# Kernel optimization log

Measured on AMD Instinct MI355X. Metric: run time of the kernel, lower is better.

Reference implementation:

```python
import jax, jax.numpy as jnp
import numpy as np
from jax import lax

EPS = 1e-5
SLOPE = 0.2

def knn_idx(x, k):
    # x: [B, C, N] -> neighbor indices [B, N, k] (largest negative sq-dist, self included)
    inner = jnp.einsum('bcn,bcm->bnm', x, x)          # [B,N,N]
    xx = jnp.sum(x * x, axis=1)                        # [B,N]
    pair = 2.0 * inner - xx[:, :, None] - xx[:, None, :]
    return lax.top_k(pair, k)[1]                       # [B,N,k]

def graph_feature(x, idx):
    # x: [B,C,N], idx: [B,N,k] -> edge features [B,N,k,2C] = (x_j - x_i, x_i)
    feat = jnp.transpose(x, (0, 2, 1))                 # [B,N,C]
    nbr = jax.vmap(lambda f, i: f[i])(feat, idx)       # [B,N,k,C]
    ctr = jnp.broadcast_to(feat[:, :, None, :], nbr.shape)
    return jnp.concatenate([nbr - ctr, ctr], axis=-1)  # [B,N,k,2C]

def bn(x, gamma, beta, axes):
    mu = jnp.mean(x, axis=axes, keepdims=True)
    var = jnp.var(x, axis=axes, keepdims=True)
    return (x - mu) * lax.rsqrt(var + EPS) * gamma + beta

def edge_conv(e, w, gamma, beta):
    # e: [B,N,k,2C], w: [O,2C] (1x1 conv, no bias) -> [B,N,O] after BN+LeakyReLU+max over k
    h = jnp.einsum('bnkc,oc->bnko', e, w)
    h = jax.nn.leaky_relu(bn(h, gamma, beta, (0, 1, 2)), SLOPE)
    return jnp.max(h, axis=2)                          # [B,N,O]

def setup_inputs() -> dict:
    key = jax.random.key(0)
    ks = jax.random.split(key, 8)
    B, C, N, O = 8, 3, 4096, 64
    x = jax.random.normal(ks[0], (B, C, N), jnp.float32)
    w_s = jax.random.normal(ks[1], (O, 2 * C), jnp.float32) * (1.0 / np.sqrt(2 * C))
    w_l = jax.random.normal(ks[2], (O, 2 * C), jnp.float32) * (1.0 / np.sqrt(2 * C))
    w_f = jax.random.normal(ks[3], (O, 2 * O), jnp.float32) * (1.0 / np.sqrt(2 * O))
    g_s = jnp.ones((O,)); b_s = jnp.zeros((O,))
    g_l = jnp.ones((O,)); b_l = jnp.zeros((O,))
    g_f = jnp.ones((O,)); b_f = jnp.zeros((O,))
    return {"x": x, "w_s": w_s, "g_s": g_s, "b_s": b_s,
            "w_l": w_l, "g_l": g_l, "b_l": b_l,
            "w_f": w_f, "g_f": g_f, "b_f": b_f}

def reference(x, w_s, g_s, b_s, w_l, g_l, b_l, w_f, g_f, b_f):
    K_SMALL, K_LARGE = 20, 40
    idx_s = knn_idx(x, K_SMALL)
    idx_l = knn_idx(x, K_LARGE)
    h_s = edge_conv(graph_feature(x, idx_s), w_s, g_s, b_s)   # [B,N,O]
    h_l = edge_conv(graph_feature(x, idx_l), w_l, g_l, b_l)   # [B,N,O]
    h = jnp.concatenate([h_s, h_l], axis=-1)                  # [B,N,2O]
    h = jnp.einsum('bnc,oc->bno', h, w_f)                     # fuse 1x1 conv
    h = jax.nn.leaky_relu(bn(h, g_f, b_f, (0, 1)), SLOPE)
    return jnp.transpose(h, (0, 2, 1))                        # [B,O,N]
```

## Files before the change

kernel.cpp:

```cpp
#include <hip/hip_runtime.h>

#define B_ 8
#define N_ 4096
#define O_ 64
#define KL 40
#define KS 20
#define EPSV 1e-5
#define SLOPE 0.2f

typedef unsigned long long u64;
typedef unsigned int u32;

__device__ __forceinline__ float leaky(float v) { return v >= 0.f ? v : SLOPE * v; }

__device__ __forceinline__ u32 mfloat(float x) {
    const u32 u = __float_as_uint(x);
    return (u & 0x80000000u) ? ~u : (u | 0x80000000u);
}
__device__ __forceinline__ float unmfloat(u32 m) {
    return __uint_as_float((m & 0x80000000u) ? (m ^ 0x80000000u) : ~m);
}

template <int S>
__device__ __forceinline__ u64 xor_ex64(u64 v, int dsaddr) {
    if constexpr (S == 1 || S == 2 || S == 8) {
        constexpr int CTRL = (S == 1) ? 0xB1 : (S == 2) ? 0x4E : 0x128;
        const int lo = __builtin_amdgcn_update_dpp(0, (int)(u32)v, CTRL, 0xF, 0xF, true);
        const int hi = __builtin_amdgcn_update_dpp(0, (int)(u32)(v >> 32), CTRL, 0xF, 0xF, true);
        return ((u64)(u32)hi << 32) | (u32)lo;
    } else {
        const int lo = __builtin_amdgcn_ds_bpermute(dsaddr, (int)(u32)v);
        const int hi = __builtin_amdgcn_ds_bpermute(dsaddr, (int)(u32)(v >> 32));
        return ((u64)(u32)hi << 32) | (u32)lo;
    }
}

template <int K, int S>
__device__ __forceinline__ void stage_pair(u64& a, u64& e, int lane, int dsaddr) {
    const u64 oa = xor_ex64<S>(a, dsaddr);
    const u64 oe = xor_ex64<S>(e, dsaddr);
    const bool sel = (((lane & K) == 0) == ((lane & S) == 0));
    a = ((a < oa) == sel) ? a : oa;
    e = ((e < oe) == sel) ? e : oe;
}

__device__ __forceinline__ void sort64_pair(u64& a, u64& e, int lane,
                                            int a4, int a16, int a32) {
    stage_pair<2, 1>(a, e, lane, 0);
    stage_pair<4, 2>(a, e, lane, 0);    stage_pair<4, 1>(a, e, lane, 0);
    stage_pair<8, 4>(a, e, lane, a4);   stage_pair<8, 2>(a, e, lane, 0);    stage_pair<8, 1>(a, e, lane, 0);
    stage_pair<16, 8>(a, e, lane, 0);   stage_pair<16, 4>(a, e, lane, a4);  stage_pair<16, 2>(a, e, lane, 0);   stage_pair<16, 1>(a, e, lane, 0);
    stage_pair<32, 16>(a, e, lane, a16); stage_pair<32, 8>(a, e, lane, 0);  stage_pair<32, 4>(a, e, lane, a4);  stage_pair<32, 2>(a, e, lane, 0);  stage_pair<32, 1>(a, e, lane, 0);
    stage_pair<64, 32>(a, e, lane, a32); stage_pair<64, 16>(a, e, lane, a16); stage_pair<64, 8>(a, e, lane, 0); stage_pair<64, 4>(a, e, lane, a4); stage_pair<64, 2>(a, e, lane, 0); stage_pair<64, 1>(a, e, lane, 0);
}

__device__ __forceinline__ void merge_pair(u64& L0, u64& L1, u64 a, u64 e, int lane,
                                           int a4, int a16, int a32, int a63) {
    const u64 ra = xor_ex64<63>(a, a63);
    const u64 re = xor_ex64<63>(e, a63);
    L0 = (L0 < ra) ? L0 : ra;
    L1 = (L1 < re) ? L1 : re;
    stage_pair<0, 32>(L0, L1, lane, a32);
    stage_pair<0, 16>(L0, L1, lane, a16);
    stage_pair<0, 8>(L0, L1, lane, 0);
    stage_pair<0, 4>(L0, L1, lane, a4);
    stage_pair<0, 2>(L0, L1, lane, 0);
    stage_pair<0, 1>(L0, L1, lane, 0);
}

__global__ __launch_bounds__(1024) void bucket_kernel(const float* __restrict__ x,
                                                      float4* __restrict__ sxp,
                                                      int* __restrict__ perm,
                                                      float2* __restrict__ cb,
                                                      float4* __restrict__ xo4) {
    __shared__ int hist[256];
    __shared__ int scan[256];
    __shared__ int ofs[256];
    __shared__ u32 xsm[4096];
    __shared__ float redmin[16], redmax[16];
    __shared__ u32 wmin[64], wmax[64];
    const int b = blockIdx.x;
    const float* xb = x + (size_t)b * 3 * N_;
    const int t = threadIdx.x;
    float xv[4];
    float mn = INFINITY, mx = -INFINITY;
#pragma unroll
    for (int p = 0; p < 4; ++p) {
        xv[p] = xb[t + p * 1024];
        mn = fminf(mn, xv[p]); mx = fmaxf(mx, xv[p]);
    }
#pragma unroll
    for (int s = 1; s < 64; s <<= 1) {
        mn = fminf(mn, __shfl_xor(mn, s));
        mx = fmaxf(mx, __shfl_xor(mx, s));
    }
    if ((t & 63) == 0) { redmin[t >> 6] = mn; redmax[t >> 6] = mx; }
    if (t < 256) hist[t] = 0;
    __syncthreads();
    if (t == 0) {
        float m0 = INFINITY, m1 = -INFINITY;
        for (int w = 0; w < 16; ++w) { m0 = fminf(m0, redmin[w]); m1 = fmaxf(m1, redmax[w]); }
        redmin[0] = m0; redmax[0] = m1;
    }
    __syncthreads();
    const float xmin = redmin[0];
    const float scale = 256.0f / fmaxf(redmax[0] - xmin, 1e-20f);
    int bk[4];
#pragma unroll
    for (int p = 0; p < 4; ++p) {
        bk[p] = min(255, max(0, (int)((xv[p] - xmin) * scale)));
        atomicAdd(&hist[bk[p]], 1);
    }
    __syncthreads();
    if (t < 256) scan[t] = hist[t];
    __syncthreads();
#pragma unroll
    for (int s = 1; s < 256; s <<= 1) {
        int v = 0;
        if (t < 256 && t >= s) v = scan[t - s];
        __syncthreads();
        if (t < 256) scan[t] += v;
        __syncthreads();
    }
    if (t < 256) ofs[t] = scan[t] - hist[t];
    if (t < 64) { wmin[t] = 0xFFFFFFFFu; wmax[t] = 0; }
    __syncthreads();
#pragma unroll
    for (int p = 0; p < 4; ++p) {
        const int i = t + p * 1024;
        const int dst = atomicAdd(&ofs[bk[p]], 1);
        const float cx = xv[p], cy = xb[N_ + i], cz = xb[2 * N_ + i];
        sxp[((size_t)b << 12) + dst] = make_float4(2.f * cx, 2.f * cy, 2.f * cz,
                                                   -(cx * cx + cy * cy + cz * cz));
        perm[(b << 12) + dst] = i;
        xo4[((size_t)b << 12) + i] = make_float4(cx, cy, cz, 0.f);
        xsm[dst] = mfloat(cx);
    }
    __syncthreads();
#pragma unroll
    for (int p = 0; p < 4; ++p) {
        const int pos = t + p * 1024;
        const int w = pos >> 6;
        atomicMin(&wmin[w], xsm[pos]);
        atomicMax(&wmax[w], xsm[pos]);
    }
    __syncthreads();
    if (t == 0) {
        u32 sm = 0xFFFFFFFFu;
        for (int w = 63; w >= 0; --w) { sm = min(sm, wmin[w]); wmin[w] = sm; }
        u32 pm2 = 0;
        for (int w = 0; w < 64; ++w) { pm2 = max(pm2, wmax[w]); wmax[w] = pm2; }
    }
    __syncthreads();
    if (t < 64) cb[(b << 6) + t] = make_float2(unmfloat(wmin[t]), unmfloat(wmax[t]));
}

__global__ __launch_bounds__(256, 8) void knn_kernel(const float4* __restrict__ sxp,
                                                     const int* __restrict__ perm,
                                                     const float2* __restrict__ cb,
                                                     const float4* __restrict__ xo4,
                                                     const float* __restrict__ w_s,
                                                     const float* __restrict__ w_l,
                                                     float* __restrict__ max_s,
                                                     float* __restrict__ min_s,
                                                     float* __restrict__ max_l,
                                                     float* __restrict__ min_l,
                                                     float* __restrict__ qstats) {
    __shared__ u64 buf[4][2][128];
    __shared__ float2 cbl[64];
    __shared__ float4 sbuf[4][2][KL];
    __shared__ float sred[4][4][64];
    const int sbid = ((blockIdx.x & 7) << 9) | (blockIdx.x >> 3);
    const int b = sbid >> 9;
    const int qbase = (sbid & 511) << 3;
    const int tid = threadIdx.x;
    const int wave = tid >> 6, lane = tid & 63;
    if (tid < 64) cbl[tid] = cb[(b << 6) + tid];
    const int a4 = (lane ^ 4) << 2, a16 = (lane ^ 16) << 2;
    const int a32 = (lane ^ 32) << 2, a63 = (lane ^ 63) << 2;
    const float4* sp = sxp + ((size_t)b << 12);
    const int* pm = perm + (b << 12);
    const float4* xo = xo4 + ((size_t)b << 12);
    const int i0 = qbase + wave * 2;
    const float4 p0 = sp[i0], p1 = sp[i0 + 1];
    const float qx0 = 0.5f * p0.x, qy0 = 0.5f * p0.y, qz0 = 0.5f * p0.z, nw0 = p0.w;
    const float qx1 = 0.5f * p1.x, qy1 = 0.5f * p1.y, qz1 = 0.5f * p1.z, nw1 = p1.w;
    const float qxmin = fminf(qx0, qx1), qxmax = fmaxf(qx0, qx1);
    int cnt0 = 0, cnt1 = 0;
    __syncthreads();
    const int home = i0 >> 6;
    u64 L0, L1;
    float th0, th1;
    {
        const int js = (home << 6) + lane;
        const float4 ch = sp[js];
        const int pj = pm[js];
        const float d0 = fmaf(qx0, ch.x, fmaf(qy0, ch.y, fmaf(qz0, ch.z, ch.w + nw0)));
        const float d1 = fmaf(qx1, ch.x, fmaf(qy1, ch.y, fmaf(qz1, ch.z, ch.w + nw1)));
        u64 k0 = ((u64)__float_as_uint(fminf(d0, -0.0f)) << 32) | (u32)pj;
        u64 k1 = ((u64)__float_as_uint(fminf(d1, -0.0f)) << 32) | (u32)pj;
        sort64_pair(k0, k1, lane, a4, a16, a32);
        L0 = k0; L1 = k1;
        th0 = __uint_as_float((u32)__builtin_amdgcn_readlane((int)(u32)(L0 >> 32), KL - 1));
        th1 = __uint_as_float((u32)__builtin_amdgcn_readlane((int)(u32)(L1 >> 32), KL - 1));
    }
    int cl = home - 1, cr = home + 1;
    bool openL = (cl >= 0), openR = (cr < 64);
    bool takeR = true;
    int c = -1;
    float4 cd = make_float4(0.f, 0.f, 0.f, 0.f);
    int pj = 0;
    for (;;) {
        if (!openL && !openR) break;
        const bool pickR = openR && (takeR || !openL);
        takeR = !pickR;
        const float r2 = -fminf(th0, th1);
        if (pickR) {
            const float dx = cbl[cr].x - qxmax;
            if (dx > 0.f && dx * dx > r2) { openR = false; continue; }
            c = cr++; if (cr >= 64) openR = false; break;
        } else {
            const float dx = qxmin - cbl[cl].y;
            if (dx > 0.f && dx * dx > r2) { openL = false; continue; }
            c = cl--; if (cl < 0) openL = false; break;
        }
    }
    if (c >= 0) { cd = sp[(c << 6) + lane]; pj = pm[(c << 6) + lane]; }
    while (c >= 0) {
        int cn = -1;
        for (;;) {
            if (!openL && !openR) break;
            const bool pickR = openR && (takeR || !openL);
            takeR = !pickR;
            const float r2 = -fminf(th0, th1);
            if (pickR) {
                const float dx = cbl[cr].x - qxmax;
                if (dx > 0.f && dx * dx > r2) { openR = false; continue; }
                cn = cr++; if (cr >= 64) openR = false; break;
            } else {
                const float dx = qxmin - cbl[cl].y;
                if (dx > 0.f && dx * dx > r2) { openL = false; continue; }
                cn = cl--; if (cl < 0) openL = false; break;
            }
        }
        float4 nd = make_float4(0.f, 0.f, 0.f, 0.f);
        int nj = 0;
        if (cn >= 0) { nd = sp[(cn << 6) + lane]; nj = pm[(cn << 6) + lane]; }
        {
            const float d0 = fmaf(qx0, cd.x, fmaf(qy0, cd.y, fmaf(qz0, cd.z, cd.w + nw0)));
            const float d1 = fmaf(qx1, cd.x, fmaf(qy1, cd.y, fmaf(qz1, cd.z, cd.w + nw1)));
            const bool pr0 = (d0 >= th0), pr1 = (d1 >= th1);
            const u64 m0 = __ballot(pr0), m1 = __ballot(pr1);
            if (m0) {
                const int pos = cnt0 + __builtin_amdgcn_mbcnt_hi(
                    (u32)(m0 >> 32), __builtin_amdgcn_mbcnt_lo((u32)m0, 0));
                if (pr0) {
                    const u32 kd = __float_as_uint(fminf(d0, -0.0f));
                    buf[wave][0][pos] = ((u64)kd << 32) | (u32)pj;
                }
                cnt0 += __popcll(m0);
            }
            if (m1) {
                const int pos = cnt1 + __builtin_amdgcn_mbcnt_hi(
                    (u32)(m1 >> 32), __builtin_amdgcn_mbcnt_lo((u32)m1, 0));
                if (pr1) {
                    const u32 kd = __float_as_uint(fminf(d1, -0.0f));
                    buf[wave][1][pos] = ((u64)kd << 32) | (u32)pj;
                }
                cnt1 += __popcll(m1);
            }
            if ((cnt0 | cnt1) >= 64) {
                const int t0 = min(cnt0, 64), t1 = min(cnt1, 64);
                u64 a = (lane < t0) ? buf[wave][0][cnt0 - t0 + lane] : ~0ull;
                u64 e = (lane < t1) ? buf[wave][1][cnt1 - t1 + lane] : ~0ull;
                sort64_pair(a, e, lane, a4, a16, a32);
                merge_pair(L0, L1, a, e, lane, a4, a16, a32, a63);
                th0 = __uint_as_float((u32)__builtin_amdgcn_readlane((int)(u32)(L0 >> 32), KL - 1));
                th1 = __uint_as_float((u32)__builtin_amdgcn_readlane((int)(u32)(L1 >> 32), KL - 1));
                cnt0 -= t0; cnt1 -= t1;
            }
        }
        c = cn; cd = nd; pj = nj;
    }
    if ((cnt0 | cnt1) > 0) {
        u64 a = (lane < cnt0) ? buf[wave][0][lane] : ~0ull;
        u64 e = (lane < cnt1) ? buf[wave][1][lane] : ~0ull;
        sort64_pair(a, e, lane, a4, a16, a32);
        merge_pair(L0, L1, a, e, lane, a4, a16, a32, a63);
    }
    if (lane < KL) {
        sbuf[wave][0][lane] = xo[(int)((u32)L0 & 4095u)];
        sbuf[wave][1][lane] = xo[(int)((u32)L1 & 4095u)];
    }
    __builtin_amdgcn_wave_barrier();
    const int lw = lane * 6;
    const float ws0 = w_s[lw], ws1 = w_s[lw + 1], ws2 = w_s[lw + 2];
    const float ds0 = w_s[lw + 3] - ws0, ds1 = w_s[lw + 4] - ws1, ds2 = w_s[lw + 5] - ws2;
    const float wl0 = w_l[lw], wl1 = w_l[lw + 1], wl2 = w_l[lw + 2];
    const float dl0 = w_l[lw + 3] - wl0, dl1 = w_l[lw + 4] - wl1, dl2 = w_l[lw + 5] - wl2;
    const int oi0 = pm[i0], oi1 = pm[i0 + 1];
    float st[4] = {0.f, 0.f, 0.f, 0.f};
#pragma unroll
    for (int q = 0; q < 2; ++q) {
        const float qx = q ? qx1 : qx0, qy = q ? qy1 : qy0, qz = q ? qz1 : qz0;
        const int oi = q ? oi1 : oi0;
        const float cs = fmaf(ds0, qx, fmaf(ds1, qy, ds2 * qz));
        const float cq = fmaf(dl0, qx, fmaf(dl1, qy, dl2 * qz));
        float mxs = -INFINITY, mns = INFINITY, mxl = -INFINITY, mnl = INFINITY;
        float sums = 0.f, sss = 0.f, suml = 0.f, ssl = 0.f;
#pragma unroll
        for (int k = 0; k < KL; ++k) {
            const float4 xj = sbuf[wave][q][k];
            const float hl = fmaf(wl0, xj.x, fmaf(wl1, xj.y, fmaf(wl2, xj.z, cq)));
            mxl = fmaxf(mxl, hl); mnl = fminf(mnl, hl);
            suml += hl; ssl = fmaf(hl, hl, ssl);
            if (k < KS) {
                const float hs = fmaf(ws0, xj.x, fmaf(ws1, xj.y, fmaf(ws2, xj.z, cs)));
                mxs = fmaxf(mxs, hs); mns = fminf(mns, hs);
                sums += hs; sss = fmaf(hs, hs, sss);
            }
        }
        const size_t base = (size_t)((b << 12) + oi) * 64 + lane;
        max_s[base] = mxs; min_s[base] = mns;
        max_l[base] = mxl; min_l[base] = mnl;
        st[0] += sums; st[1] += sss; st[2] += suml; st[3] += ssl;
    }
#pragma unroll
    for (int s = 0; s < 4; ++s) sred[wave][s][lane] = st[s];
    __syncthreads();
    if (tid < 256) {
        const int s = tid >> 6, ch = tid & 63;
        qstats[(size_t)blockIdx.x * 256 + tid] =
            sred[0][s][ch] + sred[1][s][ch] + sred[2][s][ch] + sred[3][s][ch];
    }
}

__global__ void reduce1a_kernel(const float* __restrict__ qstats, double* __restrict__ partialD1) {
    const int t = threadIdx.x;
    double acc = 0.0;
    const int r0 = blockIdx.x * 128;
    for (int r = 0; r < 128; ++r) acc += (double)qstats[(size_t)(r0 + r) * 256 + t];
    partialD1[(size_t)blockIdx.x * 256 + t] = acc;
}

__global__ void reduce1b_kernel(const double* __restrict__ partialD1,
                                const float* __restrict__ g_s, const float* __restrict__ b_s,
                                const float* __restrict__ g_l, const float* __restrict__ b_l,
                                float* __restrict__ sb1) {
    const int t = threadIdx.x;
    double acc = 0.0;
    for (int r = 0; r < 32; ++r) acc += partialD1[(size_t)r * 256 + t];
    __shared__ double sums[256];
    sums[t] = acc;
    __syncthreads();
    if (t < 64) {
        const double ns = (double)B_ * N_ * KS;
        const double nl = (double)B_ * N_ * KL;
        double mu = sums[t] / ns;
        double var = sums[64 + t] / ns - mu * mu;
        double sc = (double)g_s[t] / sqrt(var + EPSV);
        sb1[t] = (float)sc;
        sb1[64 + t] = (float)((double)b_s[t] - mu * sc);
        mu = sums[128 + t] / nl;
        var = sums[192 + t] / nl - mu * mu;
        sc = (double)g_l[t] / sqrt(var + EPSV);
        sb1[128 + t] = (float)sc;
        sb1[192 + t] = (float)((double)b_l[t] - mu * sc);
    }
}

__global__ __launch_bounds__(256) void fuse_kernel(
    const float* __restrict__ max_s, const float* __restrict__ min_s,
    const float* __restrict__ max_l, const float* __restrict__ min_l,
    const float* __restrict__ sb1, const float* __restrict__ w_f,
    float* __restrict__ f_buf, float* __restrict__ partial2) {
    __shared__ float wfT[128 * 64];
    __shared__ float av[4][128];
    __shared__ float red[2][4][64];
    const int tid = threadIdx.x;
    for (int t = tid; t < 8192; t += 256) {
        const int c = t >> 6, o = t & 63;
        wfT[t] = w_f[o * 128 + c];
    }
    const int sbid = ((blockIdx.x & 7) << 8) + (blockIdx.x >> 3);
    const int wave = tid >> 6, lane = tid & 63;
    const float sc_s = sb1[lane], bi_s = sb1[64 + lane];
    const float sc_l = sb1[128 + lane], bi_l = sb1[192 + lane];
    float sum_f = 0.f, ss_f = 0.f;
    __syncthreads();
    for (int p = 0; p < 4; ++p) {
        const int bn = (sbid * 4 + wave) * 4 + p;
        const size_t base = (size_t)bn * 64 + lane;
        const float hs = sc_s >= 0.f ? max_s[base] : min_s[base];
        const float a_s = leaky(fmaf(sc_s, hs, bi_s));
        const float hl = sc_l >= 0.f ? max_l[base] : min_l[base];
        const float a_l = leaky(fmaf(sc_l, hl, bi_l));
        av[wave][lane] = a_s;
        av[wave][64 + lane] = a_l;
        float acc = 0.f;
#pragma unroll
        for (int c = 0; c < 128; ++c) acc = fmaf(wfT[c * 64 + lane], av[wave][c], acc);
        f_buf[base] = acc;
        sum_f += acc;
        ss_f = fmaf(acc, acc, ss_f);
    }
    red[0][wave][lane] = sum_f;
    red[1][wave][lane] = ss_f;
    __syncthreads();
    if (tid < 128) {
        const int st = tid >> 6, o = tid & 63;
        partial2[(size_t)blockIdx.x * 128 + tid] =
            red[st][0][o] + red[st][1][o] + red[st][2][o] + red[st][3][o];
    }
}

__global__ void reduce2a_kernel(const float* __restrict__ partial2, double* __restrict__ partialD2) {
    const int t = threadIdx.x;
    double acc = 0.0;
    const int r0 = blockIdx.x * 32;
    for (int r = 0; r < 32; ++r) acc += (double)partial2[(size_t)(r0 + r) * 128 + t];
    partialD2[(size_t)blockIdx.x * 128 + t] = acc;
}

__global__ void reduce2b_kernel(const double* __restrict__ partialD2,
                                const float* __restrict__ g_f, const float* __restrict__ b_f,
                                float* __restrict__ sb2) {
    const int t = threadIdx.x;
    double acc = 0.0;
    for (int r = 0; r < 64; ++r) acc += partialD2[(size_t)r * 128 + t];
    __shared__ double sums[128];
    sums[t] = acc;
    __syncthreads();
    if (t < 64) {
        const double n = (double)B_ * N_;
        const double mu = sums[t] / n;
        const double var = sums[64 + t] / n - mu * mu;
        const double sc = (double)g_f[t] / sqrt(var + EPSV);
        sb2[t] = (float)sc;
        sb2[64 + t] = (float)((double)b_f[t] - mu * sc);
    }
}

__global__ __launch_bounds__(256) void final_kernel(const float* __restrict__ f_buf,
                                                    const float* __restrict__ sb2,
                                                    float* __restrict__ out) {
    __shared__ float tile[64][65];
    const int sbid = ((blockIdx.x & 7) << 6) + (blockIdx.x >> 3);
    const int b = sbid >> 6;
    const int n0 = (sbid & 63) << 6;
#pragma unroll
    for (int r = 0; r < 16; ++r) {
        const int t = r * 256 + threadIdx.x;
        const int n = t >> 6, o = t & 63;
        const float v = f_buf[(size_t)((b << 12) + n0 + n) * 64 + o];
        const float h = fmaf(sb2[o], v, sb2[64 + o]);
        tile[n][o] = leaky(h);
    }
    __syncthreads();
#pragma unroll
    for (int r = 0; r < 16; ++r) {
        const int t = r * 256 + threadIdx.x;
        const int o = t >> 6, n = t & 63;
        out[(size_t)((b << 6) + o) * N_ + n0 + n] = tile[n][o];
    }
}

extern "C" void kernel_launch(void* const* d_in, const int* in_sizes, int n_in,
                              void* d_out, int out_size, void* d_ws, size_t ws_size,
                              hipStream_t stream) {
    (void)in_sizes; (void)n_in; (void)out_size; (void)ws_size;
    const float* x   = (const float*)d_in[0];
    const float* w_s = (const float*)d_in[1];
    const float* g_s = (const float*)d_in[2];
    const float* b_s = (const float*)d_in[3];
    const float* w_l = (const float*)d_in[4];
    const float* g_l = (const float*)d_in[5];
    const float* b_l = (const float*)d_in[6];
    const float* w_f = (const float*)d_in[7];
    const float* g_f = (const float*)d_in[8];
    const float* b_f = (const float*)d_in[9];
    float* out = (float*)d_out;
    char* ws = (char*)d_ws;

    constexpr size_t SZ_PT   = (size_t)B_ * N_ * 64 * 4;
    constexpr size_t OFF_MXS = 0;
    constexpr size_t OFF_MNS = OFF_MXS + SZ_PT;
    constexpr size_t OFF_MXL = OFF_MNS + SZ_PT;
    constexpr size_t OFF_MNL = OFF_MXL + SZ_PT;
    constexpr size_t OFF_QST = OFF_MNL + SZ_PT;
    constexpr size_t OFF_PD1 = OFF_QST + (size_t)4096 * 256 * 4;
    constexpr size_t OFF_SB1 = OFF_PD1 + (size_t)32 * 256 * 8;
    constexpr size_t OFF_F   = OFF_SB1 + 1024;
    constexpr size_t OFF_P2  = OFF_F + SZ_PT;
    constexpr size_t OFF_PD2 = OFF_P2 + (size_t)2048 * 128 * 4;
    constexpr size_t OFF_SB2 = OFF_PD2 + (size_t)64 * 128 * 8;
    constexpr size_t OFF_SXP = OFF_SB2 + 1024;
    constexpr size_t OFF_PRM = OFF_SXP + (size_t)B_ * N_ * 16;
    constexpr size_t OFF_CB  = OFF_PRM + (size_t)B_ * N_ * 4;
    constexpr size_t OFF_XO4 = OFF_CB + (size_t)B_ * 64 * 8;

    float*  mxs  = (float*)(ws + OFF_MXS);
    float*  mns  = (float*)(ws + OFF_MNS);
    float*  mxl  = (float*)(ws + OFF_MXL);
    float*  mnl  = (float*)(ws + OFF_MNL);
    float*  qst  = (float*)(ws + OFF_QST);
    double* pd1  = (double*)(ws + OFF_PD1);
    float*  sb1  = (float*)(ws + OFF_SB1);
    float*  fb   = (float*)(ws + OFF_F);
    float*  p2   = (float*)(ws + OFF_P2);
    double* pd2  = (double*)(ws + OFF_PD2);
    float*  sb2  = (float*)(ws + OFF_SB2);
    float4* sxp  = (float4*)(ws + OFF_SXP);
    int*    prm  = (int*)(ws + OFF_PRM);
    float2* cbv  = (float2*)(ws + OFF_CB);
    float4* xo4  = (float4*)(ws + OFF_XO4);

    hipLaunchKernelGGL(bucket_kernel, dim3(8), dim3(1024), 0, stream, x, sxp, prm, cbv, xo4);
    hipLaunchKernelGGL(knn_kernel, dim3(4096), dim3(256), 0, stream,
                       sxp, prm, cbv, xo4, w_s, w_l, mxs, mns, mxl, mnl, qst);
    hipLaunchKernelGGL(reduce1a_kernel, dim3(32), dim3(256), 0, stream, qst, pd1);
    hipLaunchKernelGGL(reduce1b_kernel, dim3(1), dim3(256), 0, stream, pd1, g_s, b_s, g_l, b_l, sb1);
    hipLaunchKernelGGL(fuse_kernel, dim3(2048), dim3(256), 0, stream,
                       mxs, mns, mxl, mnl, sb1, w_f, fb, p2);
    hipLaunchKernelGGL(reduce2a_kernel, dim3(64), dim3(128), 0, stream, p2, pd2);
    hipLaunchKernelGGL(reduce2b_kernel, dim3(1), dim3(128), 0, stream, pd2, g_f, b_f, sb2);
    hipLaunchKernelGGL(final_kernel, dim3(512), dim3(256), 0, stream, fb, sb2, out);
}
```

Before: 197.9 us.

## Process four queries per wavefront in kNN instead of two

Each wave now handles four spatially adjacent queries rather than two. Candidate chunk loads, bucket pruning and the bitonic sort/merge DPP exchanges are shared across more queries, halving the grid and amortizing the traversal cost. The per-wave LDS buffer doubles and is reused to stage the neighbour coordinates, and launch bounds drop to 7 waves per SIMD. In exchange the union pruning radius is looser (fminf over four thresholds), so more candidates may be visited, and register pressure rises.

```diff
diff --git a/kernel.cpp b/kernel.cpp
--- a/kernel.cpp
+++ b/kernel.cpp
@@ -36,36 +36,46 @@
 }
 
 template <int K, int S>
-__device__ __forceinline__ void stage_pair(u64& a, u64& e, int lane, int dsaddr) {
+__device__ __forceinline__ void stage_quad(u64& a, u64& e, u64& f, u64& g,
+                                           int lane, int dsaddr) {
     const u64 oa = xor_ex64<S>(a, dsaddr);
     const u64 oe = xor_ex64<S>(e, dsaddr);
+    const u64 of = xor_ex64<S>(f, dsaddr);
+    const u64 og = xor_ex64<S>(g, dsaddr);
     const bool sel = (((lane & K) == 0) == ((lane & S) == 0));
     a = ((a < oa) == sel) ? a : oa;
     e = ((e < oe) == sel) ? e : oe;
-}
-
-__device__ __forceinline__ void sort64_pair(u64& a, u64& e, int lane,
+    f = ((f < of) == sel) ? f : of;
+    g = ((g < og) == sel) ? g : og;
+}
+
+__device__ __forceinline__ void sort64_quad(u64& a, u64& e, u64& f, u64& g, int lane,
                                             int a4, int a16, int a32) {
-    stage_pair<2, 1>(a, e, lane, 0);
-    stage_pair<4, 2>(a, e, lane, 0);    stage_pair<4, 1>(a, e, lane, 0);
-    stage_pair<8, 4>(a, e, lane, a4);   stage_pair<8, 2>(a, e, lane, 0);    stage_pair<8, 1>(a, e, lane, 0);
-    stage_pair<16, 8>(a, e, lane, 0);   stage_pair<16, 4>(a, e, lane, a4);  stage_pair<16, 2>(a, e, lane, 0);   stage_pair<16, 1>(a, e, lane, 0);
-    stage_pair<32, 16>(a, e, lane, a16); stage_pair<32, 8>(a, e, lane, 0);  stage_pair<32, 4>(a, e, lane, a4);  stage_pair<32, 2>(a, e, lane, 0);  stage_pair<32, 1>(a, e, lane, 0);
-    stage_pair<64, 32>(a, e, lane, a32); stage_pair<64, 16>(a, e, lane, a16); stage_pair<64, 8>(a, e, lane, 0); stage_pair<64, 4>(a, e, lane, a4); stage_pair<64, 2>(a, e, lane, 0); stage_pair<64, 1>(a, e, lane, 0);
-}
-
-__device__ __forceinline__ void merge_pair(u64& L0, u64& L1, u64 a, u64 e, int lane,
+    stage_quad<2, 1>(a, e, f, g, lane, 0);
+    stage_quad<4, 2>(a, e, f, g, lane, 0);    stage_quad<4, 1>(a, e, f, g, lane, 0);
+    stage_quad<8, 4>(a, e, f, g, lane, a4);   stage_quad<8, 2>(a, e, f, g, lane, 0);    stage_quad<8, 1>(a, e, f, g, lane, 0);
+    stage_quad<16, 8>(a, e, f, g, lane, 0);   stage_quad<16, 4>(a, e, f, g, lane, a4);  stage_quad<16, 2>(a, e, f, g, lane, 0);   stage_quad<16, 1>(a, e, f, g, lane, 0);
+    stage_quad<32, 16>(a, e, f, g, lane, a16); stage_quad<32, 8>(a, e, f, g, lane, 0);  stage_quad<32, 4>(a, e, f, g, lane, a4);  stage_quad<32, 2>(a, e, f, g, lane, 0);  stage_quad<32, 1>(a, e, f, g, lane, 0);
+    stage_quad<64, 32>(a, e, f, g, lane, a32); stage_quad<64, 16>(a, e, f, g, lane, a16); stage_quad<64, 8>(a, e, f, g, lane, 0); stage_quad<64, 4>(a, e, f, g, lane, a4); stage_quad<64, 2>(a, e, f, g, lane, 0); stage_quad<64, 1>(a, e, f, g, lane, 0);
+}
+
+__device__ __forceinline__ void merge_quad(u64& L0, u64& L1, u64& L2, u64& L3,
+                                           u64 a, u64 e, u64 f, u64 g, int lane,
                                            int a4, int a16, int a32, int a63) {
     const u64 ra = xor_ex64<63>(a, a63);
     const u64 re = xor_ex64<63>(e, a63);
+    const u64 rf = xor_ex64<63>(f, a63);
+    const u64 rg = xor_ex64<63>(g, a63);
     L0 = (L0 < ra) ? L0 : ra;
     L1 = (L1 < re) ? L1 : re;
-    stage_pair<0, 32>(L0, L1, lane, a32);
-    stage_pair<0, 16>(L0, L1, lane, a16);
-    stage_pair<0, 8>(L0, L1, lane, 0);
-    stage_pair<0, 4>(L0, L1, lane, a4);
-    stage_pair<0, 2>(L0, L1, lane, 0);
-    stage_pair<0, 1>(L0, L1, lane, 0);
+    L2 = (L2 < rf) ? L2 : rf;
+    L3 = (L3 < rg) ? L3 : rg;
+    stage_quad<0, 32>(L0, L1, L2, L3, lane, a32);
+    stage_quad<0, 16>(L0, L1, L2, L3, lane, a16);
+    stage_quad<0, 8>(L0, L1, L2, L3, lane, 0);
+    stage_quad<0, 4>(L0, L1, L2, L3, lane, a4);
+    stage_quad<0, 2>(L0, L1, L2, L3, lane, 0);
+    stage_quad<0, 1>(L0, L1, L2, L3, lane, 0);
 }
 
 __global__ __launch_bounds__(1024) void bucket_kernel(const float* __restrict__ x,
@@ -155,7 +165,7 @@
     if (t < 64) cb[(b << 6) + t] = make_float2(unmfloat(wmin[t]), unmfloat(wmax[t]));
 }
 
-__global__ __launch_bounds__(256, 8) void knn_kernel(const float4* __restrict__ sxp,
+__global__ __launch_bounds__(256, 7) void knn_kernel(const float4* __restrict__ sxp,
                                                      const int* __restrict__ perm,
                                                      const float2* __restrict__ cb,
                                                      const float4* __restrict__ xo4,
@@ -166,13 +176,12 @@
                                                      float* __restrict__ max_l,
                                                      float* __restrict__ min_l,
                                                      float* __restrict__ qstats) {
-    __shared__ u64 buf[4][2][128];
+    __shared__ u64 buf[4][4][128];
     __shared__ float2 cbl[64];
-    __shared__ float4 sbuf[4][2][KL];
     __shared__ float sred[4][4][64];
-    const int sbid = ((blockIdx.x & 7) << 9) | (blockIdx.x >> 3);
-    const int b = sbid >> 9;
-    const int qbase = (sbid & 511) << 3;
+    const int sbid = ((blockIdx.x & 7) << 8) | (blockIdx.x >> 3);
+    const int b = sbid >> 8;
+    const int qbase = (sbid & 255) << 4;
     const int tid = threadIdx.x;
     const int wave = tid >> 6, lane = tid & 63;
     if (tid < 64) cbl[tid] = cb[(b << 6) + tid];
@@ -181,28 +190,37 @@
     const float4* sp = sxp + ((size_t)b << 12);
     const int* pm = perm + (b << 12);
     const float4* xo = xo4 + ((size_t)b << 12);
-    const int i0 = qbase + wave * 2;
-    const float4 p0 = sp[i0], p1 = sp[i0 + 1];
+    const int i0 = qbase + wave * 4;
+    const float4 p0 = sp[i0], p1 = sp[i0 + 1], p2 = sp[i0 + 2], p3 = sp[i0 + 3];
     const float qx0 = 0.5f * p0.x, qy0 = 0.5f * p0.y, qz0 = 0.5f * p0.z, nw0 = p0.w;
     const float qx1 = 0.5f * p1.x, qy1 = 0.5f * p1.y, qz1 = 0.5f * p1.z, nw1 = p1.w;
-    const float qxmin = fminf(qx0, qx1), qxmax = fmaxf(qx0, qx1);
-    int cnt0 = 0, cnt1 = 0;
+    const float qx2 = 0.5f * p2.x, qy2 = 0.5f * p2.y, qz2 = 0.5f * p2.z, nw2 = p2.w;
+    const float qx3 = 0.5f * p3.x, qy3 = 0.5f * p3.y, qz3 = 0.5f * p3.z, nw3 = p3.w;
+    const float qxmin = fminf(fminf(qx0, qx1), fminf(qx2, qx3));
+    const float qxmax = fmaxf(fmaxf(qx0, qx1), fmaxf(qx2, qx3));
+    int cnt0 = 0, cnt1 = 0, cnt2 = 0, cnt3 = 0;
     __syncthreads();
     const int home = i0 >> 6;
-    u64 L0, L1;
-    float th0, th1;
+    u64 L0, L1, L2, L3;
+    float th0, th1, th2, th3;
     {
         const int js = (home << 6) + lane;
         const float4 ch = sp[js];
         const int pj = pm[js];
         const float d0 = fmaf(qx0, ch.x, fmaf(qy0, ch.y, fmaf(qz0, ch.z, ch.w + nw0)));
         const float d1 = fmaf(qx1, ch.x, fmaf(qy1, ch.y, fmaf(qz1, ch.z, ch.w + nw1)));
+        const float d2 = fmaf(qx2, ch.x, fmaf(qy2, ch.y, fmaf(qz2, ch.z, ch.w + nw2)));
+        const float d3 = fmaf(qx3, ch.x, fmaf(qy3, ch.y, fmaf(qz3, ch.z, ch.w + nw3)));
         u64 k0 = ((u64)__float_as_uint(fminf(d0, -0.0f)) << 32) | (u32)pj;
         u64 k1 = ((u64)__float_as_uint(fminf(d1, -0.0f)) << 32) | (u32)pj;
-        sort64_pair(k0, k1, lane, a4, a16, a32);
-        L0 = k0; L1 = k1;
+        u64 k2 = ((u64)__float_as_uint(fminf(d2, -0.0f)) << 32) | (u32)pj;
+        u64 k3 = ((u64)__float_as_uint(fminf(d3, -0.0f)) << 32) | (u32)pj;
+        sort64_quad(k0, k1, k2, k3, lane, a4, a16, a32);
+        L0 = k0; L1 = k1; L2 = k2; L3 = k3;
         th0 = __uint_as_float((u32)__builtin_amdgcn_readlane((int)(u32)(L0 >> 32), KL - 1));
         th1 = __uint_as_float((u32)__builtin_amdgcn_readlane((int)(u32)(L1 >> 32), KL - 1));
+        th2 = __uint_as_float((u32)__builtin_amdgcn_readlane((int)(u32)(L2 >> 32), KL - 1));
+        th3 = __uint_as_float((u32)__builtin_amdgcn_readlane((int)(u32)(L3 >> 32), KL - 1));
     }
     int cl = home - 1, cr = home + 1;
     bool openL = (cl >= 0), openR = (cr < 64);
@@ -214,7 +232,7 @@
         if (!openL && !openR) break;
         const bool pickR = openR && (takeR || !openL);
         takeR = !pickR;
-        const float r2 = -fminf(th0, th1);
+        const float r2 = -fminf(fminf(th0, th1), fminf(th2, th3));
         if (pickR) {
             const float dx = cbl[cr].x - qxmax;
             if (dx > 0.f && dx * dx > r2) { openR = false; continue; }
@@ -232,7 +250,7 @@
             if (!openL && !openR) break;
             const bool pickR = openR && (takeR || !openL);
             takeR = !pickR;
-            const float r2 = -fminf(th0, th1);
+            const float r2 = -fminf(fminf(th0, th1), fminf(th2, th3));
             if (pickR) {
                 const float dx = cbl[cr].x - qxmax;
                 if (dx > 0.f && dx * dx > r2) { openR = false; continue; }
@@ -249,48 +267,72 @@
         {
             const float d0 = fmaf(qx0, cd.x, fmaf(qy0, cd.y, fmaf(qz0, cd.z, cd.w + nw0)));
             const float d1 = fmaf(qx1, cd.x, fmaf(qy1, cd.y, fmaf(qz1, cd.z, cd.w + nw1)));
-            const bool pr0 = (d0 >= th0), pr1 = (d1 >= th1);
-            const u64 m0 = __ballot(pr0), m1 = __ballot(pr1);
+            const float d2 = fmaf(qx2, cd.x, fmaf(qy2, cd.y, fmaf(qz2, cd.z, cd.w + nw2)));
+            const float d3 = fmaf(qx3, cd.x, fmaf(qy3, cd.y, fmaf(qz3, cd.z, cd.w + nw3)));
+            const u64 m0 = __ballot(d0 >= th0);
+            const u64 m1 = __ballot(d1 >= th1);
+            const u64 m2 = __ballot(d2 >= th2);
+            const u64 m3 = __ballot(d3 >= th3);
             if (m0) {
                 const int pos = cnt0 + __builtin_amdgcn_mbcnt_hi(
                     (u32)(m0 >> 32), __builtin_amdgcn_mbcnt_lo((u32)m0, 0));
-                if (pr0) {
-                    const u32 kd = __float_as_uint(fminf(d0, -0.0f));
-                    buf[wave][0][pos] = ((u64)kd << 32) | (u32)pj;
-                }
+                if (d0 >= th0) buf[wave][0][pos] =
+                    ((u64)__float_as_uint(fminf(d0, -0.0f)) << 32) | (u32)pj;
                 cnt0 += __popcll(m0);
             }
             if (m1) {
                 const int pos = cnt1 + __builtin_amdgcn_mbcnt_hi(
                     (u32)(m1 >> 32), __builtin_amdgcn_mbcnt_lo((u32)m1, 0));
-                if (pr1) {
-                    const u32 kd = __float_as_uint(fminf(d1, -0.0f));
-                    buf[wave][1][pos] = ((u64)kd << 32) | (u32)pj;
-                }
+                if (d1 >= th1) buf[wave][1][pos] =
+                    ((u64)__float_as_uint(fminf(d1, -0.0f)) << 32) | (u32)pj;
                 cnt1 += __popcll(m1);
             }
-            if ((cnt0 | cnt1) >= 64) {
+            if (m2) {
+                const int pos = cnt2 + __builtin_amdgcn_mbcnt_hi(
+                    (u32)(m2 >> 32), __builtin_amdgcn_mbcnt_lo((u32)m2, 0));
+                if (d2 >= th2) buf[wave][2][pos] =
+                    ((u64)__float_as_uint(fminf(d2, -0.0f)) << 32) | (u32)pj;
+                cnt2 += __popcll(m2);
+            }
+            if (m3) {
+                const int pos = cnt3 + __builtin_amdgcn_mbcnt_hi(
+                    (u32)(m3 >> 32), __builtin_amdgcn_mbcnt_lo((u32)m3, 0));
+                if (d3 >= th3) buf[wave][3][pos] =
+                    ((u64)__float_as_uint(fminf(d3, -0.0f)) << 32) | (u32)pj;
+                cnt3 += __popcll(m3);
+            }
+            if ((cnt0 | cnt1 | cnt2 | cnt3) >= 64) {
                 const int t0 = min(cnt0, 64), t1 = min(cnt1, 64);
+                const int t2 = min(cnt2, 64), t3 = min(cnt3, 64);
                 u64 a = (lane < t0) ? buf[wave][0][cnt0 - t0 + lane] : ~0ull;
                 u64 e = (lane < t1) ? buf[wave][1][cnt1 - t1 + lane] : ~0ull;
-                sort64_pair(a, e, lane, a4, a16, a32);
-                merge_pair(L0, L1, a, e, lane, a4, a16, a32, a63);
+                u64 f = (lane < t2) ? buf[wave][2][cnt2 - t2 + lane] : ~0ull;
+                u64 g = (lane < t3) ? buf[wave][3][cnt3 - t3 + lane] : ~0ull;
+                sort64_quad(a, e, f, g, lane, a4, a16, a32);
+                merge_quad(L0, L1, L2, L3, a, e, f, g, lane, a4, a16, a32, a63);
                 th0 = __uint_as_float((u32)__builtin_amdgcn_readlane((int)(u32)(L0 >> 32), KL - 1));
                 th1 = __uint_as_float((u32)__builtin_amdgcn_readlane((int)(u32)(L1 >> 32), KL - 1));
-                cnt0 -= t0; cnt1 -= t1;
+                th2 = __uint_as_float((u32)__builtin_amdgcn_readlane((int)(u32)(L2 >> 32), KL - 1));
+                th3 = __uint_as_float((u32)__builtin_amdgcn_readlane((int)(u32)(L3 >> 32), KL - 1));
+                cnt0 -= t0; cnt1 -= t1; cnt2 -= t2; cnt3 -= t3;
             }
         }
         c = cn; cd = nd; pj = nj;
     }
-    if ((cnt0 | cnt1) > 0) {
+    if ((cnt0 | cnt1 | cnt2 | cnt3) > 0) {
         u64 a = (lane < cnt0) ? buf[wave][0][lane] : ~0ull;
         u64 e = (lane < cnt1) ? buf[wave][1][lane] : ~0ull;
-        sort64_pair(a, e, lane, a4, a16, a32);
-        merge_pair(L0, L1, a, e, lane, a4, a16, a32, a63);
-    }
+        u64 f = (lane < cnt2) ? buf[wave][2][lane] : ~0ull;
+        u64 g = (lane < cnt3) ? buf[wave][3][lane] : ~0ull;
+        sort64_quad(a, e, f, g, lane, a4, a16, a32);
+        merge_quad(L0, L1, L2, L3, a, e, f, g, lane, a4, a16, a32, a63);
+    }
+    float4* sbufw = reinterpret_cast<float4*>(&buf[wave][0][0]);
     if (lane < KL) {
-        sbuf[wave][0][lane] = xo[(int)((u32)L0 & 4095u)];
-        sbuf[wave][1][lane] = xo[(int)((u32)L1 & 4095u)];
+        sbufw[0 * KL + lane] = xo[(int)((u32)L0 & 4095u)];
+        sbufw[1 * KL + lane] = xo[(int)((u32)L1 & 4095u)];
+        sbufw[2 * KL + lane] = xo[(int)((u32)L2 & 4095u)];
+        sbufw[3 * KL + lane] = xo[(int)((u32)L3 & 4095u)];
     }
     __builtin_amdgcn_wave_barrier();
     const int lw = lane * 6;
@@ -298,19 +340,20 @@
     const float ds0 = w_s[lw + 3] - ws0, ds1 = w_s[lw + 4] - ws1, ds2 = w_s[lw + 5] - ws2;
     const float wl0 = w_l[lw], wl1 = w_l[lw + 1], wl2 = w_l[lw + 2];
     const float dl0 = w_l[lw + 3] - wl0, dl1 = w_l[lw + 4] - wl1, dl2 = w_l[lw + 5] - wl2;
-    const int oi0 = pm[i0], oi1 = pm[i0 + 1];
     float st[4] = {0.f, 0.f, 0.f, 0.f};
 #pragma unroll
-    for (int q = 0; q < 2; ++q) {
-        const float qx = q ? qx1 : qx0, qy = q ? qy1 : qy0, qz = q ? qz1 : qz0;
-        const int oi = q ? oi1 : oi0;
+    for (int q = 0; q < 4; ++q) {
+        const float qx = (q == 0) ? qx0 : (q == 1) ? qx1 : (q == 2) ? qx2 : qx3;
+        const float qy = (q == 0) ? qy0 : (q == 1) ? qy1 : (q == 2) ? qy2 : qy3;
+        const float qz = (q == 0) ? qz0 : (q == 1) ? qz1 : (q == 2) ? qz2 : qz3;
+        const int oi = pm[i0 + q];
         const float cs = fmaf(ds0, qx, fmaf(ds1, qy, ds2 * qz));
         const float cq = fmaf(dl0, qx, fmaf(dl1, qy, dl2 * qz));
         float mxs = -INFINITY, mns = INFINITY, mxl = -INFINITY, mnl = INFINITY;
         float sums = 0.f, sss = 0.f, suml = 0.f, ssl = 0.f;
 #pragma unroll
         for (int k = 0; k < KL; ++k) {
-            const float4 xj = sbuf[wave][q][k];
+            const float4 xj = sbufw[q * KL + k];
             const float hl = fmaf(wl0, xj.x, fmaf(wl1, xj.y, fmaf(wl2, xj.z, cq)));
             mxl = fmaxf(mxl, hl); mnl = fminf(mnl, hl);
             suml += hl; ssl = fmaf(hl, hl, ssl);
@@ -338,8 +381,8 @@
 __global__ void reduce1a_kernel(const float* __restrict__ qstats, double* __restrict__ partialD1) {
     const int t = threadIdx.x;
     double acc = 0.0;
-    const int r0 = blockIdx.x * 128;
-    for (int r = 0; r < 128; ++r) acc += (double)qstats[(size_t)(r0 + r) * 256 + t];
+    const int r0 = blockIdx.x * 64;
+    for (int r = 0; r < 64; ++r) acc += (double)qstats[(size_t)(r0 + r) * 256 + t];
     partialD1[(size_t)blockIdx.x * 256 + t] = acc;
 }
 
@@ -488,7 +531,7 @@
     constexpr size_t OFF_MXL = OFF_MNS + SZ_PT;
     constexpr size_t OFF_MNL = OFF_MXL + SZ_PT;
     constexpr size_t OFF_QST = OFF_MNL + SZ_PT;
-    constexpr size_t OFF_PD1 = OFF_QST + (size_t)4096 * 256 * 4;
+    constexpr size_t OFF_PD1 = OFF_QST + (size_t)2048 * 256 * 4;
     constexpr size_t OFF_SB1 = OFF_PD1 + (size_t)32 * 256 * 8;
     constexpr size_t OFF_F   = OFF_SB1 + 1024;
     constexpr size_t OFF_P2  = OFF_F + SZ_PT;
@@ -516,7 +559,7 @@
     float4* xo4  = (float4*)(ws + OFF_XO4);
 
     hipLaunchKernelGGL(bucket_kernel, dim3(8), dim3(1024), 0, stream, x, sxp, prm, cbv, xo4);
-    hipLaunchKernelGGL(knn_kernel, dim3(4096), dim3(256), 0, stream,
+    hipLaunchKernelGGL(knn_kernel, dim3(2048), dim3(256), 0, stream,
                        sxp, prm, cbv, xo4, w_s, w_l, mxs, mns, mxl, mnl, qst);
     hipLaunchKernelGGL(reduce1a_kernel, dim3(32), dim3(256), 0, stream, qst, pd1);
     hipLaunchKernelGGL(reduce1b_kernel, dim3(1), dim3(256), 0, stream, pd1, g_s, b_s, g_l, b_l, sb1);
```

New measurement: 240.8 us. 1.22x slower.
